# Kernel optimization log

Hardware: AMD Instinct MI355X
Metric: run time of the kernel (lower is better)

## Reference

```python
import jax, jax.numpy as jnp
import numpy as np

TEMPERATURE = 0.1


def setup_inputs() -> dict:
    key = jax.random.key(0)
    k1, k2 = jax.random.split(key)
    B, B_pos, D = 8192, 8192, 1024
    generated = jax.random.normal(k1, (B, D), dtype=jnp.float32)
    positive = jax.random.normal(k2, (B_pos, D), dtype=jnp.float32)
    return {"generated": generated, "positive": positive}


def _pairwise_dist_sq(x, y):
    # (N, M) squared L2 distances, clamped at 0
    x_norm = jnp.sum(x * x, axis=-1, keepdims=True)          # (N, 1)
    y_norm = jnp.sum(y * y, axis=-1, keepdims=True)          # (M, 1)
    d2 = x_norm + y_norm.T - 2.0 * (x @ y.T)
    return jnp.clip(d2, 0.0)


def reference(generated, positive):
    gen = generated.reshape(generated.shape[0], -1)
    pos = positive.reshape(positive.shape[0], -1)
    B = gen.shape[0]

    # Attraction: softmax over distances to positives.
    dist_pos = jnp.sqrt(_pairwise_dist_sq(gen, pos))          # (B, B_pos)
    w_pos = jax.nn.softmax(-dist_pos / TEMPERATURE, axis=1)
    # sum_j w_ij (pos_j - gen_i) == (w_pos @ pos) - gen  (rows of w sum to 1)
    attraction = w_pos @ pos - gen                            # (B, D)

    # Repulsion: softmax over distances to other generated samples (diag masked).
    d2_neg = _pairwise_dist_sq(gen, gen)
    eye = jnp.eye(B, dtype=bool)
    dist_neg = jnp.sqrt(jnp.where(eye, jnp.inf, d2_neg))      # inf diag -> weight 0
    w_neg = jax.nn.softmax(-dist_neg / TEMPERATURE, axis=1)
    repulsion = w_neg @ gen - gen                             # (B, D)

    drift = attraction - repulsion
    target = jax.lax.stop_gradient(gen + drift)
    loss = jnp.mean((gen - target) ** 2)

    drift_norm = jnp.mean(jnp.linalg.norm(drift, axis=-1))
    attraction_norm = jnp.mean(jnp.linalg.norm(attraction, axis=-1))
    repulsion_norm = jnp.mean(jnp.linalg.norm(repulsion, axis=-1))
    return (loss, drift_norm, attraction_norm, repulsion_norm)
```

## Files before the change

### kernel.cpp

```cpp
#include <hip/hip_runtime.h>
#include <stdint.h>

#define INV_T 10.0f
#define SHIFT_ 460.0f
#define MROWS 8192
#define DDIM 1024
#define CHUNK 1024

typedef __attribute__((ext_vector_type(8))) short bf16x8;
typedef __attribute__((ext_vector_type(4))) float f32x4;

__device__ __forceinline__ float bf2f(unsigned short u) {
  return __uint_as_float(((unsigned int)u) << 16);
}
__device__ __forceinline__ unsigned short f2bf(float f) {
  unsigned int u = __float_as_uint(f);
  return (unsigned short)((u + 0x7FFFu + ((u >> 16) & 1u)) >> 16);
}
__device__ __forceinline__ void gl2lds16(const unsigned short* g, unsigned short* l) {
  __builtin_amdgcn_global_load_lds((const __attribute__((address_space(1))) void*)g,
                                   (__attribute__((address_space(3))) void*)l, 16, 0, 0);
}

__global__ void prep_kernel(const float* __restrict__ gen, const float* __restrict__ pos,
                            unsigned short* __restrict__ gen_h, unsigned short* __restrict__ pos_h,
                            float* __restrict__ gn2, float* __restrict__ pn2) {
  int b = blockIdx.x;
  const float* src; unsigned short* dst; float* n2; int row;
  if (b < MROWS) { src = gen; dst = gen_h; n2 = gn2; row = b; }
  else           { src = pos; dst = pos_h; n2 = pn2; row = b - MROWS; }
  int t = threadIdx.x;
  float4 v = ((const float4*)(src + (size_t)row * DDIM))[t];
  float ss = v.x * v.x + v.y * v.y + v.z * v.z + v.w * v.w;
  ushort4 o;
  o.x = f2bf(v.x); o.y = f2bf(v.y); o.z = f2bf(v.z); o.w = f2bf(v.w);
  ((ushort4*)(dst + (size_t)row * DDIM))[t] = o;
#pragma unroll
  for (int m = 1; m < 64; m <<= 1) ss += __shfl_xor(ss, m);
  __shared__ float red[4];
  if ((t & 63) == 0) red[t >> 6] = ss;
  __syncthreads();
  if (t == 0) n2[row] = red[0] + red[1] + red[2] + red[3];
}

__global__ void transpose_kernel(const float* __restrict__ gen, const float* __restrict__ pos,
                                 unsigned short* __restrict__ genT, unsigned short* __restrict__ posT) {
  __shared__ float tile[64][65];
  int b = blockIdx.x;
  const float* src; unsigned short* dst;
  if (b < 2048) { src = gen; dst = genT; }
  else          { src = pos; dst = posT; b -= 2048; }
  int tj = b >> 4, td = b & 15;
  int t = threadIdx.x;
#pragma unroll
  for (int it = 0; it < 16; ++it) {
    int idx = it * 256 + t;
    int r = idx >> 6, c = idx & 63;
    tile[r][c] = src[(size_t)(tj * 64 + r) * DDIM + td * 64 + c];
  }
  __syncthreads();
#pragma unroll
  for (int it = 0; it < 16; ++it) {
    int idx = it * 256 + t;
    int d = idx >> 6, j = idx & 63;
    dst[(size_t)(td * 64 + d) * MROWS + tj * 64 + j] = f2bf(tile[j][d]);
  }
}

template <int EPI>
__launch_bounds__(256, 2)
__global__ void gemm_bt(const unsigned short* __restrict__ A0, const unsigned short* __restrict__ A1,
                        long lda,
                        const unsigned short* __restrict__ B0, const unsigned short* __restrict__ B1,
                        long ldb, int ksteps,
                        unsigned short* __restrict__ P0, unsigned short* __restrict__ P1,
                        int pld, int j0,
                        const float* __restrict__ qn2,
                        const float* __restrict__ kn2a, const float* __restrict__ kn2b,
                        float* __restrict__ lsum0, float* __restrict__ lsum1,
                        unsigned short* __restrict__ O0, unsigned short* __restrict__ O1,
                        int first) {
  __shared__ __align__(16) unsigned short Al[128 * 64];
  __shared__ __align__(16) unsigned short Bl[128 * 64];

  const int NXB = gridDim.x, NYB = gridDim.y;
  const int nwg = NXB * NYB * gridDim.z;
  const int orig = blockIdx.x + NXB * (blockIdx.y + NYB * blockIdx.z);
  const int wid = (orig & 7) * (nwg >> 3) + (orig >> 3);
  const int by = wid % NYB;
  const int bx = (wid / NYB) % NXB;
  const int bz = wid / (NYB * NXB);

  const int z = bz;
  const unsigned short* A = z ? A1 : A0;
  const unsigned short* B = z ? B1 : B0;
  const int t = threadIdx.x;
  const int w = t >> 6, lane = t & 63, l15 = lane & 15, quad = lane >> 4;
  const int wm = w >> 1, wn = w & 1;
  const long m0 = (long)bx * 128;
  const long n0 = (long)by * 128;
  const int trow = t >> 3;
  const int tcol = (((t & 7) ^ (trow & 7)) * 8);

  f32x4 acc[4][4];
#pragma unroll
  for (int i = 0; i < 4; ++i)
#pragma unroll
    for (int j = 0; j < 4; ++j) acc[i][j] = (f32x4){0.f, 0.f, 0.f, 0.f};

  const unsigned short* Ab = A + (m0 + trow) * lda + tcol;
  const unsigned short* Bb = B + (n0 + trow) * ldb + tcol;
  unsigned short* Alw = Al + t * 8;
  unsigned short* Blw = Bl + t * 8;
  const int ue = (quad ^ (l15 & 7)) * 8;

  for (int ks = 0; ks < ksteps; ++ks) {
    const long ko = (long)ks * 64;
#pragma unroll
    for (int i = 0; i < 4; ++i) gl2lds16(Ab + (long)i * 32 * lda + ko, Alw + i * 2048);
#pragma unroll
    for (int i = 0; i < 4; ++i) gl2lds16(Bb + (long)i * 32 * ldb + ko, Blw + i * 2048);
    __syncthreads();
#pragma unroll
    for (int kk = 0; kk < 2; ++kk) {
      const int uo = ue ^ (kk * 32);
      bf16x8 af[4], bfr[4];
#pragma unroll
      for (int mi = 0; mi < 4; ++mi)
        af[mi] = *(const bf16x8*)(Al + (wm * 64 + mi * 16 + l15) * 64 + uo);
#pragma unroll
      for (int ni = 0; ni < 4; ++ni)
        bfr[ni] = *(const bf16x8*)(Bl + (wn * 64 + ni * 16 + l15) * 64 + uo);
#pragma unroll
      for (int mi = 0; mi < 4; ++mi)
#pragma unroll
        for (int ni = 0; ni < 4; ++ni)
          acc[mi][ni] = __builtin_amdgcn_mfma_f32_16x16x32_bf16(af[mi], bfr[ni], acc[mi][ni], 0, 0, 0);
    }
    __syncthreads();
  }

  if (EPI == 0) {
    unsigned short* Pout = z ? P1 : P0;
    const float* kn2 = z ? kn2b : kn2a;
    float* lsum = z ? lsum1 : lsum0;
#pragma unroll
    for (int mi = 0; mi < 4; ++mi) {
      float rs[4] = {0.f, 0.f, 0.f, 0.f};
#pragma unroll
      for (int ni = 0; ni < 4; ++ni) {
        int c = (int)n0 + wn * 64 + ni * 16 + l15;
        float kn = kn2[j0 + c];
#pragma unroll
        for (int reg = 0; reg < 4; ++reg) {
          long r = m0 + wm * 64 + mi * 16 + quad * 4 + reg;
          float v = acc[mi][ni][reg];
          float d2 = qn2[r] + kn - 2.0f * v;
          float p = __expf(SHIFT_ - INV_T * sqrtf(fmaxf(d2, 0.0f)));
          if (z && (int)r == (j0 + c)) p = 0.0f;
          rs[reg] += p;
          Pout[r * (long)pld + c] = f2bf(p);
        }
      }
#pragma unroll
      for (int reg = 0; reg < 4; ++reg) {
        float v = rs[reg];
        v += __shfl_xor(v, 1); v += __shfl_xor(v, 2);
        v += __shfl_xor(v, 4); v += __shfl_xor(v, 8);
        if (l15 == 0) atomicAdd(&lsum[m0 + wm * 64 + mi * 16 + quad * 4 + reg], v);
      }
    }
  } else {
    unsigned short* Oh = z ? O1 : O0;
#pragma unroll
    for (int mi = 0; mi < 4; ++mi)
#pragma unroll
      for (int ni = 0; ni < 4; ++ni) {
        long c = n0 + wn * 64 + ni * 16 + l15;
#pragma unroll
        for (int reg = 0; reg < 4; ++reg) {
          long r = m0 + wm * 64 + mi * 16 + quad * 4 + reg;
          long off = r * DDIM + c;
          float v = acc[mi][ni][reg];
          Oh[off] = f2bf(first ? v : (bf2f(Oh[off]) + v));
        }
      }
  }
}

__global__ void epi_kernel(const unsigned short* __restrict__ OA, const unsigned short* __restrict__ OR_,
                           const float* __restrict__ lsumA, const float* __restrict__ lsumR,
                           const float* __restrict__ genf, float* __restrict__ gs) {
  __shared__ float wsL[4], wsD[4], wsA[4], wsR[4];
  const int t = threadIdx.x;
  const int w = t >> 6;
  const int lane = t & 63;
  float accL = 0.f, accD = 0.f, accA = 0.f, accR = 0.f;

  for (int i = 0; i < 8; ++i) {
    const int row = blockIdx.x * 32 + w * 8 + i;
    const float invlA = 1.0f / lsumA[row];
    const float invlR = 1.0f / lsumR[row];
    float ssA = 0.f, ssR = 0.f, ssD = 0.f;
#pragma unroll
    for (int u = 0; u < 4; ++u) {
      const long off = (long)row * DDIM + u * 256 + lane * 4;
      float4 g = *(const float4*)(genf + off);
      ushort4 oa = *(const ushort4*)(OA + off);
      ushort4 orr = *(const ushort4*)(OR_ + off);
      float g4[4] = {g.x, g.y, g.z, g.w};
      float a4[4] = {bf2f(oa.x), bf2f(oa.y), bf2f(oa.z), bf2f(oa.w)};
      float r4[4] = {bf2f(orr.x), bf2f(orr.y), bf2f(orr.z), bf2f(orr.w)};
#pragma unroll
      for (int e = 0; e < 4; ++e) {
        float a_ = a4[e] * invlA - g4[e];
        float r_ = r4[e] * invlR - g4[e];
        float d_ = a_ - r_;
        ssA += a_ * a_; ssR += r_ * r_; ssD += d_ * d_;
      }
    }
#pragma unroll
    for (int m = 1; m < 64; m <<= 1) {
      ssA += __shfl_xor(ssA, m);
      ssR += __shfl_xor(ssR, m);
      ssD += __shfl_xor(ssD, m);
    }
    accA += sqrtf(ssA); accR += sqrtf(ssR); accD += sqrtf(ssD); accL += ssD;
  }
  if (lane == 0) { wsL[w] = accL; wsD[w] = accD; wsA[w] = accA; wsR[w] = accR; }
  __syncthreads();
  if (t == 0) {
    atomicAdd(&gs[0], wsL[0] + wsL[1] + wsL[2] + wsL[3]);
    atomicAdd(&gs[1], wsD[0] + wsD[1] + wsD[2] + wsD[3]);
    atomicAdd(&gs[2], wsA[0] + wsA[1] + wsA[2] + wsA[3]);
    atomicAdd(&gs[3], wsR[0] + wsR[1] + wsR[2] + wsR[3]);
  }
}

__global__ void finalize_kernel(const float* __restrict__ gs, float* __restrict__ out) {
  int t = threadIdx.x;
  if (t == 0) out[0] = gs[0] / (8192.0f * 1024.0f);
  if (t == 1) out[1] = gs[1] / 8192.0f;
  if (t == 2) out[2] = gs[2] / 8192.0f;
  if (t == 3) out[3] = gs[3] / 8192.0f;
}

extern "C" void kernel_launch(void* const* d_in, const int* in_sizes, int n_in,
                              void* d_out, int out_size, void* d_ws, size_t ws_size,
                              hipStream_t stream) {
  const float* gen = (const float*)d_in[0];
  const float* pos = (const float*)d_in[1];
  char* ws = (char*)d_ws;
  const size_t MB = (size_t)1 << 20;
  unsigned short* gen_h = (unsigned short*)(ws + 0 * MB);
  unsigned short* pos_h = (unsigned short*)(ws + 16 * MB);
  unsigned short* genT  = (unsigned short*)(ws + 32 * MB);
  unsigned short* posT  = (unsigned short*)(ws + 48 * MB);
  unsigned short* Pa    = (unsigned short*)(ws + 64 * MB);
  unsigned short* Pr    = (unsigned short*)(ws + 80 * MB);
  unsigned short* OhA   = (unsigned short*)(ws + 96 * MB);
  unsigned short* OhR   = (unsigned short*)(ws + 112 * MB);
  float* gn2   = (float*)(ws + 128 * MB);
  float* pn2   = (float*)(ws + 128 * MB + 32768);
  float* lsumA = (float*)(ws + 128 * MB + 65536);
  float* lsumR = (float*)(ws + 128 * MB + 98304);
  float* gs    = (float*)(ws + 128 * MB + 131072);

  hipMemsetAsync(gs, 0, 4 * sizeof(float), stream);
  hipMemsetAsync(lsumA, 0, 2 * MROWS * sizeof(float), stream);
  prep_kernel<<<dim3(16384), dim3(256), 0, stream>>>(gen, pos, gen_h, pos_h, gn2, pn2);
  transpose_kernel<<<dim3(4096), dim3(256), 0, stream>>>(gen, pos, genT, posT);

  const int nchunks = MROWS / CHUNK;
  for (int c = 0; c < nchunks; ++c) {
    const int j0 = c * CHUNK;
    gemm_bt<0><<<dim3(64, CHUNK / 128, 2), dim3(256), 0, stream>>>(
        gen_h, gen_h, DDIM,
        pos_h + (long)j0 * DDIM, gen_h + (long)j0 * DDIM, DDIM, DDIM / 64,
        Pa, Pr, CHUNK, j0, gn2, pn2, gn2, lsumA, lsumR, nullptr, nullptr, 0);
    gemm_bt<1><<<dim3(64, DDIM / 128, 2), dim3(256), 0, stream>>>(
        Pa, Pr, CHUNK,
        posT + j0, genT + j0, MROWS, CHUNK / 64,
        nullptr, nullptr, 0, 0, nullptr, nullptr, nullptr, nullptr, nullptr,
        OhA, OhR, c == 0);
  }

  epi_kernel<<<dim3(256), dim3(256), 0, stream>>>(OhA, OhR, lsumA, lsumR, gen, gs);
  finalize_kernel<<<dim3(1), dim3(64), 0, stream>>>(gs, (float*)d_out);
}
```

Before: 932.1 us.

## Run full-width score and PV GEMMs in single launches when workspace allows

When the workspace holds the full 8192x8192 bf16 probability matrices, the chunked loop of 16 small GEMM launches becomes one score GEMM over all columns and one PV GEMM with K=8192. The score GEMM also gets an 8x8 tile-grouped block swizzle for better L2 reuse. This removes per-chunk launch gaps and tail effects, and the second GEMM no longer reloads and accumulates partial outputs. In exchange it needs about 256 MB more scratch and writes and reads the whole P matrix through memory at once. If the workspace is too small, the old chunked path still runs.

```diff
diff --git a/kernel.cpp b/kernel.cpp
--- a/kernel.cpp
+++ b/kernel.cpp
@@ -87,9 +87,18 @@
   const int nwg = NXB * NYB * gridDim.z;
   const int orig = blockIdx.x + NXB * (blockIdx.y + NYB * blockIdx.z);
   const int wid = (orig & 7) * (nwg >> 3) + (orig >> 3);
-  const int by = wid % NYB;
-  const int bx = (wid / NYB) % NXB;
-  const int bz = wid / (NYB * NXB);
+  int bx, by, bz;
+  if (NYB == 64) {
+    bz = wid >> 12;
+    const int r2 = wid & 4095;
+    const int st = r2 >> 6, i = r2 & 63;
+    bx = (st & 7) * 8 + (i & 7);
+    by = (st >> 3) * 8 + (i >> 3);
+  } else {
+    by = wid % NYB;
+    bx = (wid / NYB) % NXB;
+    bz = wid / (NYB * NXB);
+  }
 
   const int z = bz;
   const unsigned short* A = z ? A1 : A0;
@@ -252,39 +261,75 @@
   const float* pos = (const float*)d_in[1];
   char* ws = (char*)d_ws;
   const size_t MB = (size_t)1 << 20;
-  unsigned short* gen_h = (unsigned short*)(ws + 0 * MB);
-  unsigned short* pos_h = (unsigned short*)(ws + 16 * MB);
-  unsigned short* genT  = (unsigned short*)(ws + 32 * MB);
-  unsigned short* posT  = (unsigned short*)(ws + 48 * MB);
-  unsigned short* Pa    = (unsigned short*)(ws + 64 * MB);
-  unsigned short* Pr    = (unsigned short*)(ws + 80 * MB);
-  unsigned short* OhA   = (unsigned short*)(ws + 96 * MB);
-  unsigned short* OhR   = (unsigned short*)(ws + 112 * MB);
-  float* gn2   = (float*)(ws + 128 * MB);
-  float* pn2   = (float*)(ws + 128 * MB + 32768);
-  float* lsumA = (float*)(ws + 128 * MB + 65536);
-  float* lsumR = (float*)(ws + 128 * MB + 98304);
-  float* gs    = (float*)(ws + 128 * MB + 131072);
-
-  hipMemsetAsync(gs, 0, 4 * sizeof(float), stream);
-  hipMemsetAsync(lsumA, 0, 2 * MROWS * sizeof(float), stream);
-  prep_kernel<<<dim3(16384), dim3(256), 0, stream>>>(gen, pos, gen_h, pos_h, gn2, pn2);
-  transpose_kernel<<<dim3(4096), dim3(256), 0, stream>>>(gen, pos, genT, posT);
-
-  const int nchunks = MROWS / CHUNK;
-  for (int c = 0; c < nchunks; ++c) {
-    const int j0 = c * CHUNK;
-    gemm_bt<0><<<dim3(64, CHUNK / 128, 2), dim3(256), 0, stream>>>(
+  const size_t need_fused = 352 * MB + 4 * 32768 + 64;
+
+  if (ws_size >= need_fused) {
+    unsigned short* gen_h = (unsigned short*)(ws + 0 * MB);
+    unsigned short* pos_h = (unsigned short*)(ws + 16 * MB);
+    unsigned short* genT  = (unsigned short*)(ws + 32 * MB);
+    unsigned short* posT  = (unsigned short*)(ws + 48 * MB);
+    unsigned short* Pa    = (unsigned short*)(ws + 64 * MB);
+    unsigned short* Pr    = (unsigned short*)(ws + 192 * MB);
+    unsigned short* OhA   = (unsigned short*)(ws + 320 * MB);
+    unsigned short* OhR   = (unsigned short*)(ws + 336 * MB);
+    float* gn2   = (float*)(ws + 352 * MB);
+    float* pn2   = (float*)(ws + 352 * MB + 32768);
+    float* lsumA = (float*)(ws + 352 * MB + 65536);
+    float* lsumR = (float*)(ws + 352 * MB + 98304);
+    float* gs    = (float*)(ws + 352 * MB + 131072);
+
+    hipMemsetAsync(gs, 0, 4 * sizeof(float), stream);
+    hipMemsetAsync(lsumA, 0, 2 * MROWS * sizeof(float), stream);
+    prep_kernel<<<dim3(16384), dim3(256), 0, stream>>>(gen, pos, gen_h, pos_h, gn2, pn2);
+    transpose_kernel<<<dim3(4096), dim3(256), 0, stream>>>(gen, pos, genT, posT);
+
+    gemm_bt<0><<<dim3(64, 64, 2), dim3(256), 0, stream>>>(
         gen_h, gen_h, DDIM,
-        pos_h + (long)j0 * DDIM, gen_h + (long)j0 * DDIM, DDIM, DDIM / 64,
-        Pa, Pr, CHUNK, j0, gn2, pn2, gn2, lsumA, lsumR, nullptr, nullptr, 0);
+        pos_h, gen_h, DDIM, DDIM / 64,
+        Pa, Pr, MROWS , 0 , gn2, pn2, gn2, lsumA, lsumR, nullptr, nullptr, 0);
     gemm_bt<1><<<dim3(64, DDIM / 128, 2), dim3(256), 0, stream>>>(
-        Pa, Pr, CHUNK,
-        posT + j0, genT + j0, MROWS, CHUNK / 64,
+        Pa, Pr, MROWS,
+        posT, genT, MROWS, MROWS / 64,
         nullptr, nullptr, 0, 0, nullptr, nullptr, nullptr, nullptr, nullptr,
-        OhA, OhR, c == 0);
-  }
-
-  epi_kernel<<<dim3(256), dim3(256), 0, stream>>>(OhA, OhR, lsumA, lsumR, gen, gs);
-  finalize_kernel<<<dim3(1), dim3(64), 0, stream>>>(gs, (float*)d_out);
-}
+        OhA, OhR, 1);
+
+    epi_kernel<<<dim3(256), dim3(256), 0, stream>>>(OhA, OhR, lsumA, lsumR, gen, gs);
+    finalize_kernel<<<dim3(1), dim3(64), 0, stream>>>(gs, (float*)d_out);
+  } else {
+    unsigned short* gen_h = (unsigned short*)(ws + 0 * MB);
+    unsigned short* pos_h = (unsigned short*)(ws + 16 * MB);
+    unsigned short* genT  = (unsigned short*)(ws + 32 * MB);
+    unsigned short* posT  = (unsigned short*)(ws + 48 * MB);
+    unsigned short* Pa    = (unsigned short*)(ws + 64 * MB);
+    unsigned short* Pr    = (unsigned short*)(ws + 80 * MB);
+    unsigned short* OhA   = (unsigned short*)(ws + 96 * MB);
+    unsigned short* OhR   = (unsigned short*)(ws + 112 * MB);
+    float* gn2   = (float*)(ws + 128 * MB);
+    float* pn2   = (float*)(ws + 128 * MB + 32768);
+    float* lsumA = (float*)(ws + 128 * MB + 65536);
+    float* lsumR = (float*)(ws + 128 * MB + 98304);
+    float* gs    = (float*)(ws + 128 * MB + 131072);
+
+    hipMemsetAsync(gs, 0, 4 * sizeof(float), stream);
+    hipMemsetAsync(lsumA, 0, 2 * MROWS * sizeof(float), stream);
+    prep_kernel<<<dim3(16384), dim3(256), 0, stream>>>(gen, pos, gen_h, pos_h, gn2, pn2);
+    transpose_kernel<<<dim3(4096), dim3(256), 0, stream>>>(gen, pos, genT, posT);
+
+    const int nchunks = MROWS / CHUNK;
+    for (int c = 0; c < nchunks; ++c) {
+      const int j0 = c * CHUNK;
+      gemm_bt<0><<<dim3(64, CHUNK / 128, 2), dim3(256), 0, stream>>>(
+          gen_h, gen_h, DDIM,
+          pos_h + (long)j0 * DDIM, gen_h + (long)j0 * DDIM, DDIM, DDIM / 64,
+          Pa, Pr, CHUNK, j0, gn2, pn2, gn2, lsumA, lsumR, nullptr, nullptr, 0);
+      gemm_bt<1><<<dim3(64, DDIM / 128, 2), dim3(256), 0, stream>>>(
+          Pa, Pr, CHUNK,
+          posT + j0, genT + j0, MROWS, CHUNK / 64,
+          nullptr, nullptr, 0, 0, nullptr, nullptr, nullptr, nullptr, nullptr,
+          OhA, OhR, c == 0);
+    }
+
+    epi_kernel<<<dim3(256), dim3(256), 0, stream>>>(OhA, OhR, lsumA, lsumR, gen, gs);
+    finalize_kernel<<<dim3(1), dim3(64), 0, stream>>>(gs, (float*)d_out);
+  }
+}
```

After: 909.7 us. 1.02x faster.

## Merge score GEMM and PV GEMM into one launch with software-pipelined chunks

Applied to the files above, without the earlier changes.

Replaces the templated GEMM with a single kernel whose blocks take one of two roles by grid-y index. Each launch computes exp scores for chunk c while doing the P·V accumulation for chunk c-1, using double-buffered P buffers. This halves the launch count and lets the two phases fill the GPU together, removing the tail and underfill of the separate smaller launches. It needs more workspace and falls back to a sequential path when the workspace is too small.

```diff
diff --git a/kernel.cpp b/kernel.cpp
--- a/kernel.cpp
+++ b/kernel.cpp
@@ -67,19 +67,21 @@
   }
 }
 
-template <int EPI>
 __launch_bounds__(256, 2)
-__global__ void gemm_bt(const unsigned short* __restrict__ A0, const unsigned short* __restrict__ A1,
-                        long lda,
-                        const unsigned short* __restrict__ B0, const unsigned short* __restrict__ B1,
-                        long ldb, int ksteps,
-                        unsigned short* __restrict__ P0, unsigned short* __restrict__ P1,
-                        int pld, int j0,
-                        const float* __restrict__ qn2,
-                        const float* __restrict__ kn2a, const float* __restrict__ kn2b,
-                        float* __restrict__ lsum0, float* __restrict__ lsum1,
-                        unsigned short* __restrict__ O0, unsigned short* __restrict__ O1,
-                        int first) {
+__global__ void gemm_mrg(int roleSplit,
+                         const unsigned short* __restrict__ Aa,
+                         const unsigned short* __restrict__ Ba0,
+                         const unsigned short* __restrict__ Ba1,
+                         unsigned short* __restrict__ Pout0, unsigned short* __restrict__ Pout1,
+                         int j0A,
+                         const float* __restrict__ qn2,
+                         const float* __restrict__ kn2a, const float* __restrict__ kn2b,
+                         float* __restrict__ lsumA, float* __restrict__ lsumR,
+                         const unsigned short* __restrict__ Pin0, const unsigned short* __restrict__ Pin1,
+                         const unsigned short* __restrict__ Vt0,
+                         const unsigned short* __restrict__ Vt1,
+                         unsigned short* __restrict__ O0, unsigned short* __restrict__ O1,
+                         int first) {
   __shared__ __align__(16) unsigned short Al[128 * 64];
   __shared__ __align__(16) unsigned short Bl[128 * 64];
 
@@ -87,18 +89,25 @@
   const int nwg = NXB * NYB * gridDim.z;
   const int orig = blockIdx.x + NXB * (blockIdx.y + NYB * blockIdx.z);
   const int wid = (orig & 7) * (nwg >> 3) + (orig >> 3);
-  const int by = wid % NYB;
+  const int gy = wid % NYB;
   const int bx = (wid / NYB) % NXB;
   const int bz = wid / (NYB * NXB);
 
   const int z = bz;
-  const unsigned short* A = z ? A1 : A0;
-  const unsigned short* B = z ? B1 : B0;
+  const int role = (gy < roleSplit) ? 0 : 1;
+  const int byl = role ? (gy - roleSplit) : gy;
+
+  const unsigned short* A;
+  const unsigned short* B;
+  long lda, ldb;
+  if (role == 0) { A = Aa;               B = z ? Ba1 : Ba0; lda = DDIM;  ldb = DDIM;  }
+  else           { A = z ? Pin1 : Pin0;  B = z ? Vt1 : Vt0; lda = CHUNK; ldb = MROWS; }
+
   const int t = threadIdx.x;
   const int w = t >> 6, lane = t & 63, l15 = lane & 15, quad = lane >> 4;
   const int wm = w >> 1, wn = w & 1;
   const long m0 = (long)bx * 128;
-  const long n0 = (long)by * 128;
+  const long n0 = (long)byl * 128;
   const int trow = t >> 3;
   const int tcol = (((t & 7) ^ (trow & 7)) * 8);
 
@@ -114,7 +123,7 @@
   unsigned short* Blw = Bl + t * 8;
   const int ue = (quad ^ (l15 & 7)) * 8;
 
-  for (int ks = 0; ks < ksteps; ++ks) {
+  for (int ks = 0; ks < DDIM / 64; ++ks) {
     const long ko = (long)ks * 64;
 #pragma unroll
     for (int i = 0; i < 4; ++i) gl2lds16(Ab + (long)i * 32 * lda + ko, Alw + i * 2048);
@@ -140,26 +149,26 @@
     __syncthreads();
   }
 
-  if (EPI == 0) {
-    unsigned short* Pout = z ? P1 : P0;
+  if (role == 0) {
+    unsigned short* Pout = z ? Pout1 : Pout0;
     const float* kn2 = z ? kn2b : kn2a;
-    float* lsum = z ? lsum1 : lsum0;
+    float* lsum = z ? lsumR : lsumA;
 #pragma unroll
     for (int mi = 0; mi < 4; ++mi) {
       float rs[4] = {0.f, 0.f, 0.f, 0.f};
 #pragma unroll
       for (int ni = 0; ni < 4; ++ni) {
         int c = (int)n0 + wn * 64 + ni * 16 + l15;
-        float kn = kn2[j0 + c];
+        float kn = kn2[j0A + c];
 #pragma unroll
         for (int reg = 0; reg < 4; ++reg) {
           long r = m0 + wm * 64 + mi * 16 + quad * 4 + reg;
           float v = acc[mi][ni][reg];
           float d2 = qn2[r] + kn - 2.0f * v;
           float p = __expf(SHIFT_ - INV_T * sqrtf(fmaxf(d2, 0.0f)));
-          if (z && (int)r == (j0 + c)) p = 0.0f;
+          if (z && (int)r == (j0A + c)) p = 0.0f;
           rs[reg] += p;
-          Pout[r * (long)pld + c] = f2bf(p);
+          Pout[r * (long)CHUNK + c] = f2bf(p);
         }
       }
 #pragma unroll
@@ -252,39 +261,81 @@
   const float* pos = (const float*)d_in[1];
   char* ws = (char*)d_ws;
   const size_t MB = (size_t)1 << 20;
-  unsigned short* gen_h = (unsigned short*)(ws + 0 * MB);
-  unsigned short* pos_h = (unsigned short*)(ws + 16 * MB);
-  unsigned short* genT  = (unsigned short*)(ws + 32 * MB);
-  unsigned short* posT  = (unsigned short*)(ws + 48 * MB);
-  unsigned short* Pa    = (unsigned short*)(ws + 64 * MB);
-  unsigned short* Pr    = (unsigned short*)(ws + 80 * MB);
-  unsigned short* OhA   = (unsigned short*)(ws + 96 * MB);
-  unsigned short* OhR   = (unsigned short*)(ws + 112 * MB);
-  float* gn2   = (float*)(ws + 128 * MB);
-  float* pn2   = (float*)(ws + 128 * MB + 32768);
-  float* lsumA = (float*)(ws + 128 * MB + 65536);
-  float* lsumR = (float*)(ws + 128 * MB + 98304);
-  float* gs    = (float*)(ws + 128 * MB + 131072);
-
-  hipMemsetAsync(gs, 0, 4 * sizeof(float), stream);
-  hipMemsetAsync(lsumA, 0, 2 * MROWS * sizeof(float), stream);
-  prep_kernel<<<dim3(16384), dim3(256), 0, stream>>>(gen, pos, gen_h, pos_h, gn2, pn2);
-  transpose_kernel<<<dim3(4096), dim3(256), 0, stream>>>(gen, pos, genT, posT);
-
-  const int nchunks = MROWS / CHUNK;
-  for (int c = 0; c < nchunks; ++c) {
-    const int j0 = c * CHUNK;
-    gemm_bt<0><<<dim3(64, CHUNK / 128, 2), dim3(256), 0, stream>>>(
-        gen_h, gen_h, DDIM,
-        pos_h + (long)j0 * DDIM, gen_h + (long)j0 * DDIM, DDIM, DDIM / 64,
-        Pa, Pr, CHUNK, j0, gn2, pn2, gn2, lsumA, lsumR, nullptr, nullptr, 0);
-    gemm_bt<1><<<dim3(64, DDIM / 128, 2), dim3(256), 0, stream>>>(
-        Pa, Pr, CHUNK,
-        posT + j0, genT + j0, MROWS, CHUNK / 64,
-        nullptr, nullptr, 0, 0, nullptr, nullptr, nullptr, nullptr, nullptr,
-        OhA, OhR, c == 0);
-  }
-
-  epi_kernel<<<dim3(256), dim3(256), 0, stream>>>(OhA, OhR, lsumA, lsumR, gen, gs);
-  finalize_kernel<<<dim3(1), dim3(64), 0, stream>>>(gs, (float*)d_out);
-}
+  const size_t need_pipe = 160 * MB + 4 * 32768 + 64;
+
+  if (ws_size >= need_pipe) {
+    unsigned short* gen_h = (unsigned short*)(ws + 0 * MB);
+    unsigned short* pos_h = (unsigned short*)(ws + 16 * MB);
+    unsigned short* genT  = (unsigned short*)(ws + 32 * MB);
+    unsigned short* posT  = (unsigned short*)(ws + 48 * MB);
+    unsigned short* Pa[2] = {(unsigned short*)(ws + 64 * MB),  (unsigned short*)(ws + 80 * MB)};
+    unsigned short* Pr[2] = {(unsigned short*)(ws + 96 * MB),  (unsigned short*)(ws + 112 * MB)};
+    unsigned short* OhA   = (unsigned short*)(ws + 128 * MB);
+    unsigned short* OhR   = (unsigned short*)(ws + 144 * MB);
+    float* gn2   = (float*)(ws + 160 * MB);
+    float* pn2   = (float*)(ws + 160 * MB + 32768);
+    float* lsumA = (float*)(ws + 160 * MB + 65536);
+    float* lsumR = (float*)(ws + 160 * MB + 98304);
+    float* gs    = (float*)(ws + 160 * MB + 131072);
+
+    hipMemsetAsync(gs, 0, 4 * sizeof(float), stream);
+    hipMemsetAsync(lsumA, 0, 2 * MROWS * sizeof(float), stream);
+    prep_kernel<<<dim3(16384), dim3(256), 0, stream>>>(gen, pos, gen_h, pos_h, gn2, pn2);
+    transpose_kernel<<<dim3(4096), dim3(256), 0, stream>>>(gen, pos, genT, posT);
+
+    const int nchunks = MROWS / CHUNK;
+    gemm_mrg<<<dim3(64, 8, 2), dim3(256), 0, stream>>>(
+        8, gen_h, pos_h, gen_h, Pa[0], Pr[0], 0, gn2, pn2, gn2, lsumA, lsumR,
+        Pa[0], Pr[0], posT, genT, OhA, OhR, 0);
+    for (int c = 1; c < nchunks; ++c) {
+      const int j0A = c * CHUNK, j0B = (c - 1) * CHUNK;
+      gemm_mrg<<<dim3(64, 16, 2), dim3(256), 0, stream>>>(
+          8, gen_h, pos_h + (long)j0A * DDIM, gen_h + (long)j0A * DDIM,
+          Pa[c & 1], Pr[c & 1], j0A, gn2, pn2, gn2, lsumA, lsumR,
+          Pa[(c - 1) & 1], Pr[(c - 1) & 1], posT + j0B, genT + j0B, OhA, OhR, (c == 1));
+    }
+    {
+      const int c = nchunks - 1;
+      gemm_mrg<<<dim3(64, 8, 2), dim3(256), 0, stream>>>(
+          0, gen_h, pos_h, gen_h, Pa[c & 1], Pr[c & 1], 0, gn2, pn2, gn2, lsumA, lsumR,
+          Pa[c & 1], Pr[c & 1], posT + (long)c * CHUNK, genT + (long)c * CHUNK, OhA, OhR, 0);
+    }
+
+    epi_kernel<<<dim3(256), dim3(256), 0, stream>>>(OhA, OhR, lsumA, lsumR, gen, gs);
+    finalize_kernel<<<dim3(1), dim3(64), 0, stream>>>(gs, (float*)d_out);
+  } else {
+    unsigned short* gen_h = (unsigned short*)(ws + 0 * MB);
+    unsigned short* pos_h = (unsigned short*)(ws + 16 * MB);
+    unsigned short* genT  = (unsigned short*)(ws + 32 * MB);
+    unsigned short* posT  = (unsigned short*)(ws + 48 * MB);
+    unsigned short* Pa    = (unsigned short*)(ws + 64 * MB);
+    unsigned short* Pr    = (unsigned short*)(ws + 80 * MB);
+    unsigned short* OhA   = (unsigned short*)(ws + 96 * MB);
+    unsigned short* OhR   = (unsigned short*)(ws + 112 * MB);
+    float* gn2   = (float*)(ws + 128 * MB);
+    float* pn2   = (float*)(ws + 128 * MB + 32768);
+    float* lsumA = (float*)(ws + 128 * MB + 65536);
+    float* lsumR = (float*)(ws + 128 * MB + 98304);
+    float* gs    = (float*)(ws + 128 * MB + 131072);
+
+    hipMemsetAsync(gs, 0, 4 * sizeof(float), stream);
+    hipMemsetAsync(lsumA, 0, 2 * MROWS * sizeof(float), stream);
+    prep_kernel<<<dim3(16384), dim3(256), 0, stream>>>(gen, pos, gen_h, pos_h, gn2, pn2);
+    transpose_kernel<<<dim3(4096), dim3(256), 0, stream>>>(gen, pos, genT, posT);
+
+    const int nchunks = MROWS / CHUNK;
+    for (int c = 0; c < nchunks; ++c) {
+      const int j0 = c * CHUNK;
+      gemm_mrg<<<dim3(64, 8, 2), dim3(256), 0, stream>>>(
+          8, gen_h, pos_h + (long)j0 * DDIM, gen_h + (long)j0 * DDIM,
+          Pa, Pr, j0, gn2, pn2, gn2, lsumA, lsumR,
+          Pa, Pr, posT, genT, OhA, OhR, 0);
+      gemm_mrg<<<dim3(64, 8, 2), dim3(256), 0, stream>>>(
+          0, gen_h, pos_h, gen_h, Pa, Pr, 0, gn2, pn2, gn2, lsumA, lsumR,
+          Pa, Pr, posT + j0, genT + j0, OhA, OhR, (c == 0));
+    }
+
+    epi_kernel<<<dim3(256), dim3(256), 0, stream>>>(OhA, OhR, lsumA, lsumR, gen, gs);
+    finalize_kernel<<<dim3(1), dim3(64), 0, stream>>>(gs, (float*)d_out);
+  }
+}
```

Result: faster. 895.0 us (-4.0%).
